# Kernel optimization log

Measured on AMD Instinct MI355X. Metric: run time of the kernel, lower is better.

## Reference

```python
import jax, jax.numpy as jnp
import numpy as np

GROUPSIZE = 128
IN_FEATURES = 4096
OUT_FEATURES = 11008
K_BLOCKS = IN_FEATURES // GROUPSIZE  # 32
M_TOKENS = 512


def setup_inputs() -> dict:
    key = jax.random.key(0)
    k1, k2, k3, k4 = jax.random.split(key, 4)
    x = jax.random.normal(k1, (M_TOKENS, IN_FEATURES), dtype=jnp.float32)
    # packed 4-bit weights: (N, K_blocks, groupsize/2) bytes, two nibbles per byte
    qweight = jax.random.randint(k2, (OUT_FEATURES, K_BLOCKS, GROUPSIZE // 2), 0, 256, dtype=jnp.int32)
    # flat per-(n, k_block) scales, size K_blocks * N
    scales = jax.random.uniform(k3, (K_BLOCKS * OUT_FEATURES,), dtype=jnp.float32) * 0.01 + 0.001
    # flat packed zero points, size K_blocks * N / 2 bytes
    qzeros = jax.random.randint(k4, (K_BLOCKS * OUT_FEATURES // 2,), 0, 256, dtype=jnp.int32)
    return {"x": x, "qweight": qweight, "scales": scales, "qzeros": qzeros}


def _dequantize_4bit(qweight, scales, qzeros):
    # qweight: (N, Kb, gs/2) int32 bytes -> unpack low nibble first, then high
    lo = qweight & 15
    hi = (qweight >> 4) & 15
    w_int = jnp.stack([lo, hi], axis=-1).reshape(OUT_FEATURES, K_BLOCKS, GROUPSIZE)
    # qzeros: flat bytes -> interleaved nibbles -> (N, Kb)
    z = jnp.stack([qzeros & 15, (qzeros >> 4) & 15], axis=-1).reshape(OUT_FEATURES, K_BLOCKS)
    s = scales.reshape(OUT_FEATURES, K_BLOCKS)
    # (q - z) * s, blockwise
    w = (w_int - z[:, :, None]).astype(s.dtype) * s[:, :, None]
    return w.reshape(OUT_FEATURES, IN_FEATURES)  # (N, K)


def reference(x, qweight, scales, qzeros):
    fp_weight = _dequantize_4bit(qweight, scales, qzeros)  # (N, K)
    return x @ fp_weight.T  # (M, N)
```

## Files before the change

### kernel.cpp

```cpp
#include <hip/hip_runtime.h>
#include <hip/hip_fp16.h>

#define M_TOK 512
#define N_OUT 11008
#define K_IN  4096
#define KB    32

typedef _Float16 f16x8 __attribute__((ext_vector_type(8)));
typedef _Float16 f16x2 __attribute__((ext_vector_type(2)));
typedef float    f32x4 __attribute__((ext_vector_type(4)));

__global__ __launch_bounds__(256) void cvt_x_kernel(const float* __restrict__ x,
                                                    _Float16* __restrict__ xh) {
    int i = (blockIdx.x * 256 + threadIdx.x) * 8;
    float4 a = *(const float4*)(x + i);
    float4 b = *(const float4*)(x + i + 4);
    f16x8 v;
    v[0] = (_Float16)a.x; v[1] = (_Float16)a.y; v[2] = (_Float16)a.z; v[3] = (_Float16)a.w;
    v[4] = (_Float16)b.x; v[5] = (_Float16)b.y; v[6] = (_Float16)b.z; v[7] = (_Float16)b.w;
    *(f16x8*)(xh + i) = v;
}

__device__ __forceinline__ void gload_lds16(const void* g, void* l) {
    __builtin_amdgcn_global_load_lds(
        (const __attribute__((address_space(1))) void*)g,
        (__attribute__((address_space(3))) void*)l,
        16, 0, 0);
}

__device__ __forceinline__ unsigned int dq_pair(int b, f16x2 fz2, f16x2 ss2) {
    unsigned int u = ((unsigned int)b & 15u) |
                     (((unsigned int)b << 12) & 0xF0000u) |
                     0x64006400u;
    f16x2 h = __builtin_bit_cast(f16x2, u);
    f16x2 w = (h - fz2) * ss2;
    return __builtin_bit_cast(unsigned int, w);
}

__global__ __launch_bounds__(256, 4)
void gemm_w4_kernel(const int* __restrict__ qw,
                    const float* __restrict__ scales,
                    const int* __restrict__ qz,
                    const _Float16* __restrict__ xh,
                    float* __restrict__ out) {
    __shared__ __align__(16) char As[128 * 128];
    __shared__ __align__(16) char Bs[64 * 128];

    const int hw  = blockIdx.x;
    const int logical = (hw & 7) * 86 + (hw >> 3);
    const int mx = logical & 3;
    const int ny = logical >> 2;

    const int n0 = ny * 64;
    const int m0 = mx * 128;

    const int tid  = threadIdx.x;
    const int lane = tid & 63;
    const int wid  = tid >> 6;
    const int wm   = wid >> 1;
    const int wn   = wid & 1;
    const int r16  = lane & 15;
    const int g4   = lane >> 4;

    const char* xbytes = (const char*)xh;
    const char* asrc[4];
#pragma unroll
    for (int i = 0; i < 4; ++i) {
        int row = (tid >> 3) + i * 32;
        int cb  = (tid & 7) * 16;
        int cbl = cb ^ ((row & 7) << 4);
        asrc[i] = xbytes + (size_t)(m0 + row) * (K_IN * 2) + cbl;
    }

    const int n_loc = tid >> 2;
    const int q     = tid & 3;
    const int n_g   = n0 + n_loc;
    const int4* qbase = (const int4*)qw + ((size_t)n_g * 512 + q * 2);
    const int fbase = n_g * KB;
    unsigned int waddr[2];
#pragma unroll
    for (int j = 0; j < 2; ++j) {
        int kt2 = q * 32 + j * 16;
        waddr[j] = n_loc * 128 + (kt2 ^ ((n_loc & 7) << 4));
    }

    f32x4 acc[4][2];
#pragma unroll
    for (int mi = 0; mi < 4; ++mi)
#pragma unroll
        for (int ni = 0; ni < 2; ++ni)
            acc[mi][ni] = (f32x4){0.f, 0.f, 0.f, 0.f};

#pragma unroll 2
    for (int it = 0; it < K_IN / 64; ++it) {
        int4 qv0 = qbase[it * 8 + 0];
        int4 qv1 = qbase[it * 8 + 1];

        const int f  = fbase + (it >> 1);
        const float s  = scales[f];
        const int  zb  = qz[f >> 1];
        const int  z   = (zb >> ((f & 1) * 4)) & 15;
        const _Float16 sh = (_Float16)s;
        const _Float16 fzh = (_Float16)(float)(1024 + z);
        const f16x2 ss2 = (f16x2){sh, sh};
        const f16x2 fz2 = (f16x2){fzh, fzh};

        __syncthreads();

#pragma unroll
        for (int i = 0; i < 4; ++i)
            gload_lds16(asrc[i] + it * 128, As + (wid * 64 + i * 256) * 16);

        {
            uint4 w;
            w.x = dq_pair(qv0.x, fz2, ss2); w.y = dq_pair(qv0.y, fz2, ss2);
            w.z = dq_pair(qv0.z, fz2, ss2); w.w = dq_pair(qv0.w, fz2, ss2);
            *(uint4*)(Bs + waddr[0]) = w;
            w.x = dq_pair(qv1.x, fz2, ss2); w.y = dq_pair(qv1.y, fz2, ss2);
            w.z = dq_pair(qv1.z, fz2, ss2); w.w = dq_pair(qv1.w, fz2, ss2);
            *(uint4*)(Bs + waddr[1]) = w;
        }

        __syncthreads();

#pragma unroll
        for (int kh = 0; kh < 2; ++kh) {
            f16x8 af[4], bf[2];
#pragma unroll
            for (int mi = 0; mi < 4; ++mi) {
                int row = wm * 64 + mi * 16 + r16;
                int off = row * 128 + ((kh * 64 + g4 * 16) ^ ((row & 7) << 4));
                af[mi] = *(const f16x8*)(As + off);
            }
#pragma unroll
            for (int ni = 0; ni < 2; ++ni) {
                int row = wn * 32 + ni * 16 + r16;
                int off = row * 128 + ((kh * 64 + g4 * 16) ^ ((row & 7) << 4));
                bf[ni] = *(const f16x8*)(Bs + off);
            }
#pragma unroll
            for (int mi = 0; mi < 4; ++mi)
#pragma unroll
                for (int ni = 0; ni < 2; ++ni)
                    acc[mi][ni] = __builtin_amdgcn_mfma_f32_16x16x32_f16(
                        af[mi], bf[ni], acc[mi][ni], 0, 0, 0);
        }
    }

#pragma unroll
    for (int mi = 0; mi < 4; ++mi) {
#pragma unroll
        for (int ni = 0; ni < 2; ++ni) {
            const int col   = n0 + wn * 32 + ni * 16 + r16;
            const int rbase = m0 + wm * 64 + mi * 16 + g4 * 4;
            f32x4 v = acc[mi][ni];
#pragma unroll
            for (int r = 0; r < 4; ++r)
                out[(size_t)(rbase + r) * N_OUT + col] = v[r];
        }
    }
}

extern "C" void kernel_launch(void* const* d_in, const int* in_sizes, int n_in,
                              void* d_out, int out_size, void* d_ws, size_t ws_size,
                              hipStream_t stream) {
    const float* x  = (const float*)d_in[0];
    const int*   qw = (const int*)d_in[1];
    const float* sc = (const float*)d_in[2];
    const int*   qz = (const int*)d_in[3];
    _Float16*    xh = (_Float16*)d_ws;
    float*       out = (float*)d_out;

    cvt_x_kernel<<<dim3((M_TOK * K_IN) / (256 * 8)), 256, 0, stream>>>(x, xh);

    gemm_w4_kernel<<<dim3(688), 256, 0, stream>>>(qw, sc, qz, xh, out);
}
```

Baseline: 233.8 us.

## Double-buffer activation tiles and dequantize weights directly into MFMA registers

Each lane now loads the packed 4-bit weights for exactly the B fragment it feeds to MFMA and dequantizes them in registers, so the B shared-memory tile and its store/load round trip go away. Activation tiles are double-buffered in LDS, and the next iteration's activations, weights and scales/zeros are prefetched while the current tile is computed, leaving one barrier per iteration instead of two. Wave pairs that share an N slice now both dequantize the same weights redundantly, and the extra prefetch registers lower the launch-bounds occupancy target from 4 to 3 blocks.

After: 282.6 us. 1.21x slower.

```diff
diff --git a/kernel.cpp b/kernel.cpp
--- a/kernel.cpp
+++ b/kernel.cpp
@@ -4,11 +4,11 @@
 #define M_TOK 512
 #define N_OUT 11008
 #define K_IN  4096
-#define KB    32
 
 typedef _Float16 f16x8 __attribute__((ext_vector_type(8)));
 typedef _Float16 f16x2 __attribute__((ext_vector_type(2)));
 typedef float    f32x4 __attribute__((ext_vector_type(4)));
+typedef unsigned int u32x4 __attribute__((ext_vector_type(4)));
 
 __global__ __launch_bounds__(256) void cvt_x_kernel(const float* __restrict__ x,
                                                     _Float16* __restrict__ xh) {
@@ -28,23 +28,22 @@
         16, 0, 0);
 }
 
-__device__ __forceinline__ unsigned int dq_pair(int b, f16x2 fz2, f16x2 ss2) {
-    unsigned int u = ((unsigned int)b & 15u) |
-                     (((unsigned int)b << 12) & 0xF0000u) |
+__device__ __forceinline__ unsigned int dq_pair(unsigned int b, f16x2 fz2, f16x2 ss2) {
+    unsigned int u = (b & 15u) |
+                     ((b << 12) & 0xF0000u) |
                      0x64006400u;
     f16x2 h = __builtin_bit_cast(f16x2, u);
     f16x2 w = (h - fz2) * ss2;
     return __builtin_bit_cast(unsigned int, w);
 }
 
-__global__ __launch_bounds__(256, 4)
+__global__ __launch_bounds__(256, 3)
 void gemm_w4_kernel(const int* __restrict__ qw,
                     const float* __restrict__ scales,
                     const int* __restrict__ qz,
                     const _Float16* __restrict__ xh,
                     float* __restrict__ out) {
-    __shared__ __align__(16) char As[128 * 128];
-    __shared__ __align__(16) char Bs[64 * 128];
+    __shared__ __align__(16) char As[2][16384];
 
     const int hw  = blockIdx.x;
     const int logical = (hw & 7) * 86 + (hw >> 3);
@@ -72,16 +71,41 @@
         asrc[i] = xbytes + (size_t)(m0 + row) * (K_IN * 2) + cbl;
     }
 
-    const int n_loc = tid >> 2;
-    const int q     = tid & 3;
-    const int n_g   = n0 + n_loc;
-    const int4* qbase = (const int4*)qw + ((size_t)n_g * 512 + q * 2);
-    const int fbase = n_g * KB;
-    unsigned int waddr[2];
-#pragma unroll
-    for (int j = 0; j < 2; ++j) {
-        int kt2 = q * 32 + j * 16;
-        waddr[j] = n_loc * 128 + (kt2 ^ ((n_loc & 7) << 4));
+    unsigned aoff[4][2];
+#pragma unroll
+    for (int mi = 0; mi < 4; ++mi) {
+        int row = wm * 64 + mi * 16 + r16;
+#pragma unroll
+        for (int kh = 0; kh < 2; ++kh)
+            aoff[mi][kh] = row * 128 + (((kh << 6) | (g4 << 4)) ^ ((row & 7) << 4));
+    }
+
+    const int nrow0 = n0 + wn * 32 + r16;
+    const int nrow1 = nrow0 + 16;
+    const int4* qrow0 = (const int4*)qw + (size_t)nrow0 * 512;
+    const int4* qrow1 = (const int4*)qw + (size_t)nrow1 * 512;
+
+    float s_pf0 = scales[nrow0 * 32];
+    float s_pf1 = scales[nrow1 * 32];
+    int   z_pf0 = qz[nrow0 * 16] & 15;
+    int   z_pf1 = qz[nrow1 * 16] & 15;
+
+    int4 qv_cur[2][2], qv_nxt[2][2];
+#pragma unroll
+    for (int kh = 0; kh < 2; ++kh) {
+        qv_cur[0][kh] = qrow0[kh * 4 + g4];
+        qv_cur[1][kh] = qrow1[kh * 4 + g4];
+    }
+#pragma unroll
+    for (int i = 0; i < 4; ++i)
+        gload_lds16(asrc[i], &As[0][(wid * 64 + i * 256) * 16]);
+
+    f16x2 ss2[2], fz2[2];
+    {
+        _Float16 sh0 = (_Float16)s_pf0, sh1 = (_Float16)s_pf1;
+        _Float16 fz0 = (_Float16)(float)(1024 + z_pf0), fz1 = (_Float16)(float)(1024 + z_pf1);
+        ss2[0] = (f16x2){sh0, sh0}; ss2[1] = (f16x2){sh1, sh1};
+        fz2[0] = (f16x2){fz0, fz0}; fz2[1] = (f16x2){fz1, fz1};
     }
 
     f32x4 acc[4][2];
@@ -91,59 +115,74 @@
         for (int ni = 0; ni < 2; ++ni)
             acc[mi][ni] = (f32x4){0.f, 0.f, 0.f, 0.f};
 
+    __syncthreads();
+
 #pragma unroll 2
-    for (int it = 0; it < K_IN / 64; ++it) {
-        int4 qv0 = qbase[it * 8 + 0];
-        int4 qv1 = qbase[it * 8 + 1];
-
-        const int f  = fbase + (it >> 1);
-        const float s  = scales[f];
-        const int  zb  = qz[f >> 1];
-        const int  z   = (zb >> ((f & 1) * 4)) & 15;
-        const _Float16 sh = (_Float16)s;
-        const _Float16 fzh = (_Float16)(float)(1024 + z);
-        const f16x2 ss2 = (f16x2){sh, sh};
-        const f16x2 fz2 = (f16x2){fzh, fzh};
-
-        __syncthreads();
-
-#pragma unroll
-        for (int i = 0; i < 4; ++i)
-            gload_lds16(asrc[i] + it * 128, As + (wid * 64 + i * 256) * 16);
-
-        {
-            uint4 w;
-            w.x = dq_pair(qv0.x, fz2, ss2); w.y = dq_pair(qv0.y, fz2, ss2);
-            w.z = dq_pair(qv0.z, fz2, ss2); w.w = dq_pair(qv0.w, fz2, ss2);
-            *(uint4*)(Bs + waddr[0]) = w;
-            w.x = dq_pair(qv1.x, fz2, ss2); w.y = dq_pair(qv1.y, fz2, ss2);
-            w.z = dq_pair(qv1.z, fz2, ss2); w.w = dq_pair(qv1.w, fz2, ss2);
-            *(uint4*)(Bs + waddr[1]) = w;
-        }
-
-        __syncthreads();
+    for (int it = 0; it < 64; ++it) {
+        const int buf = it & 1;
+
+        if (it < 63) {
+#pragma unroll
+            for (int i = 0; i < 4; ++i)
+                gload_lds16(asrc[i] + (it + 1) * 128, &As[buf ^ 1][(wid * 64 + i * 256) * 16]);
+#pragma unroll
+            for (int kh = 0; kh < 2; ++kh) {
+                qv_nxt[0][kh] = qrow0[(it + 1) * 8 + kh * 4 + g4];
+                qv_nxt[1][kh] = qrow1[(it + 1) * 8 + kh * 4 + g4];
+            }
+        }
+        if (((it & 1) == 0) && (it < 62)) {
+            const int g = (it >> 1) + 1;
+            const int f0 = nrow0 * 32 + g, f1 = nrow1 * 32 + g;
+            s_pf0 = scales[f0];
+            s_pf1 = scales[f1];
+            z_pf0 = (qz[f0 >> 1] >> ((f0 & 1) * 4)) & 15;
+            z_pf1 = (qz[f1 >> 1] >> ((f1 & 1) * 4)) & 15;
+        }
+
+        f16x8 bf[2][2];
+#pragma unroll
+        for (int ni = 0; ni < 2; ++ni) {
+#pragma unroll
+            for (int kh = 0; kh < 2; ++kh) {
+                const int4 v = qv_cur[ni][kh];
+                u32x4 t;
+                t.x = dq_pair((unsigned)v.x, fz2[ni], ss2[ni]);
+                t.y = dq_pair((unsigned)v.y, fz2[ni], ss2[ni]);
+                t.z = dq_pair((unsigned)v.z, fz2[ni], ss2[ni]);
+                t.w = dq_pair((unsigned)v.w, fz2[ni], ss2[ni]);
+                bf[ni][kh] = __builtin_bit_cast(f16x8, t);
+            }
+        }
 
 #pragma unroll
         for (int kh = 0; kh < 2; ++kh) {
-            f16x8 af[4], bf[2];
-#pragma unroll
-            for (int mi = 0; mi < 4; ++mi) {
-                int row = wm * 64 + mi * 16 + r16;
-                int off = row * 128 + ((kh * 64 + g4 * 16) ^ ((row & 7) << 4));
-                af[mi] = *(const f16x8*)(As + off);
-            }
-#pragma unroll
-            for (int ni = 0; ni < 2; ++ni) {
-                int row = wn * 32 + ni * 16 + r16;
-                int off = row * 128 + ((kh * 64 + g4 * 16) ^ ((row & 7) << 4));
-                bf[ni] = *(const f16x8*)(Bs + off);
-            }
+            f16x8 af[4];
+#pragma unroll
+            for (int mi = 0; mi < 4; ++mi)
+                af[mi] = *(const f16x8*)(&As[buf][0] + aoff[mi][kh]);
 #pragma unroll
             for (int mi = 0; mi < 4; ++mi)
 #pragma unroll
                 for (int ni = 0; ni < 2; ++ni)
                     acc[mi][ni] = __builtin_amdgcn_mfma_f32_16x16x32_f16(
-                        af[mi], bf[ni], acc[mi][ni], 0, 0, 0);
+                        af[mi], bf[ni][kh], acc[mi][ni], 0, 0, 0);
+        }
+
+        __syncthreads();
+
+        if (it < 63) {
+#pragma unroll
+            for (int kh = 0; kh < 2; ++kh) {
+                qv_cur[0][kh] = qv_nxt[0][kh];
+                qv_cur[1][kh] = qv_nxt[1][kh];
+            }
+        }
+        if (((it & 1) == 1) && (it < 63)) {
+            _Float16 sh0 = (_Float16)s_pf0, sh1 = (_Float16)s_pf1;
+            _Float16 fz0 = (_Float16)(float)(1024 + z_pf0), fz1 = (_Float16)(float)(1024 + z_pf1);
+            ss2[0] = (f16x2){sh0, sh0}; ss2[1] = (f16x2){sh1, sh1};
+            fz2[0] = (f16x2){fz0, fz0}; fz2[1] = (f16x2){fz1, fz1};
         }
     }
 
```
